# Performance work log

Hardware: AMD Instinct MI355X
Metric: run time of the kernel (lower is better)

## Reference

```python
import jax, jax.numpy as jnp
import numpy as np

B, H, W, C = 16, 56, 56, 384
NH, WIN = 8, 7
HD2 = C // NH // 2  # per-head k/v dim (=24)
SCALE = HD2 ** -0.5

def _ln(x, w, b, eps=1e-6):
    m = x.mean(-1, keepdims=True)
    v = ((x - m) ** 2).mean(-1, keepdims=True)
    return (x - m) / jnp.sqrt(v + eps) * w + b

def _dwconv(x, w, b):
    # x: [B,C,H,W], w: [C,1,7,7], groups=C depthwise, padding 3
    y = jax.lax.conv_general_dilated(x, w, (1, 1), [(3, 3), (3, 3)],
        dimension_numbers=('NCHW', 'OIHW', 'NCHW'), feature_group_count=x.shape[1])
    return y + b[None, :, None, None]

def setup_inputs():
    key = jax.random.key(0)
    ks = iter(jax.random.split(key, 32))
    def lin(i, o):
        return jax.random.normal(next(ks), (i, o), jnp.float32) * 0.02
    C2 = C // 2
    return dict(
        x=jax.random.normal(next(ks), (B, H, W, C), jnp.float32),
        x_e=jax.random.normal(next(ks), (B, H, W, C2), jnp.float32),
        norm_w=jnp.ones((C,), jnp.float32), norm_b=jnp.zeros((C,), jnp.float32),
        norme_w=jnp.ones((C2,), jnp.float32), norme_b=jnp.zeros((C2,), jnp.float32),
        q_w=lin(C, C), q_b=jnp.zeros((C,), jnp.float32),
        qcut_w=lin(C, C2), qcut_b=jnp.zeros((C2,), jnp.float32),
        a_w=lin(C, C), a_b=jnp.zeros((C,), jnp.float32),
        l_w=lin(C, C), l_b=jnp.zeros((C,), jnp.float32),
        conv_w=jax.random.normal(next(ks), (C, 1, 7, 7), jnp.float32) * 0.02,
        conv_b=jnp.zeros((C,), jnp.float32),
        econv_w=jax.random.normal(next(ks), (C2, 1, 7, 7), jnp.float32) * 0.02,
        econv_b=jnp.zeros((C2,), jnp.float32),
        efore_w=lin(C2, C2), efore_b=jnp.zeros((C2,), jnp.float32),
        eback_w=lin(C2, C2), eback_b=jnp.zeros((C2,), jnp.float32),
        kv_w=lin(C, C), kv_b=jnp.zeros((C,), jnp.float32),
        scl_w=lin(3 * C2, C2), scl_b=jnp.zeros((C2,), jnp.float32),
        proj_w=lin(2 * C, C), proj_b=jnp.zeros((C,), jnp.float32),
        proje_w=lin(2 * C, C2), proje_b=jnp.zeros((C2,), jnp.float32),
    )

def reference(x, x_e, norm_w, norm_b, norme_w, norme_b, q_w, q_b, qcut_w, qcut_b,
              a_w, a_b, l_w, l_b, conv_w, conv_b, econv_w, econv_b,
              efore_w, efore_b, eback_w, eback_b, kv_w, kv_b, scl_w, scl_b,
              proj_w, proj_b, proje_w, proje_b):
    C2 = C // 2
    xn = _ln(x, norm_w, norm_b)
    xen = _ln(x_e, norme_w, norme_b)
    # pooled shortcut queries: AdaptiveAvgPool2d((7,7)) == uniform 8x8 mean since H=W=56
    sc = jnp.concatenate([xn, xen], -1).transpose(0, 3, 1, 2)          # [B,3C/2,H,W]
    pooled = sc.reshape(B, 3 * C2, WIN, H // WIN, WIN, W // WIN).mean((3, 5))
    pooled = pooled.transpose(0, 2, 3, 1)                               # [B,7,7,3C/2]
    m = (pooled @ scl_w + scl_b).reshape(B, WIN * WIN, NH, HD2).transpose(0, 2, 1, 3)
    q = xn @ q_w + q_b
    cut = xn @ qcut_w + qcut_b
    lx = jax.nn.gelu(xn @ l_w + l_b, approximate=False)                 # [B,H,W,C]
    a = _dwconv(lx.transpose(0, 3, 1, 2), conv_w, conv_b).transpose(0, 2, 3, 1) @ a_w + a_b
    kv = (lx.reshape(B, H * W, C) @ kv_w + kv_b).reshape(B, H * W, 2, NH, HD2)
    k = kv[:, :, 0].transpose(0, 2, 1, 3)                               # [B,NH,HW,HD2]
    v = kv[:, :, 1].transpose(0, 2, 1, 3)
    p = jax.nn.softmax(jnp.einsum('bnqd,bnkd->bnqk', m * SCALE, k), -1) # [B,NH,49,HW]
    o = jnp.einsum('bnqk,bnkd->bnqd', p, v)                             # [B,NH,49,HD2]
    o = o.reshape(B, NH, WIN, WIN, HD2).transpose(0, 1, 4, 2, 3).reshape(B, C2, WIN, WIN)
    attn = jax.image.resize(o, (B, C2, H, W), method='bilinear').transpose(0, 2, 3, 1)
    # x_e depthwise branch
    ef = xen @ efore_w + efore_b
    xe2 = _dwconv(ef.transpose(0, 3, 1, 2), econv_w, econv_b).transpose(0, 2, 3, 1) @ eback_w + eback_b
    cut = cut * xe2
    g = q * a
    cat = jnp.concatenate([g, attn, cut], -1)                           # [B,H,W,2C]
    x_e_out = cat @ proje_w + proje_b
    x_out = cat @ proj_w + proj_b
    return (x_out, x_e_out)
```

## Files before the change

### kernel.cpp

```cpp
#include <hip/hip_runtime.h>
#include <math.h>

#define NB 16
#define NHW 3136
#define NROWS 50176
#define CD 384
#define CH2 192
#define SCL 0.20412414523193154f

typedef short bf16x8 __attribute__((ext_vector_type(8)));
typedef float f32x4 __attribute__((ext_vector_type(4)));
typedef unsigned short ushort;

static __device__ __forceinline__ float gelu_exact(float v) {
  return 0.5f * v * (1.0f + erff(v * 0.70710678118654752440f));
}
static __device__ __forceinline__ ushort f2bf(float f) {
  unsigned u = __builtin_bit_cast(unsigned, f);
  u += 0x7fffu + ((u >> 16) & 1u);
  return (ushort)(u >> 16);
}
static __device__ __forceinline__ float bf2f(ushort h) {
  unsigned u = ((unsigned)h) << 16;
  return __builtin_bit_cast(float, u);
}

template<int CN>
__global__ __launch_bounds__(256) void ln_k(const float* __restrict__ x,
    const float* __restrict__ w, const float* __restrict__ b,
    ushort* __restrict__ oh, ushort* __restrict__ ol)
{
  constexpr int NPER = CN / 64;
  int wave = threadIdx.x >> 6, lane = threadIdx.x & 63;
  int row = blockIdx.x * 4 + wave;
  const float* xp = x + (size_t)row * CN;
  float v[NPER];
  float s = 0.f;
  #pragma unroll
  for (int i = 0; i < NPER; i++) { v[i] = xp[lane + 64*i]; s += v[i]; }
  #pragma unroll
  for (int off = 32; off; off >>= 1) s += __shfl_xor(s, off);
  float mean = s * (1.0f / CN);
  float vs = 0.f;
  #pragma unroll
  for (int i = 0; i < NPER; i++) { float d = v[i] - mean; vs += d*d; }
  #pragma unroll
  for (int off = 32; off; off >>= 1) vs += __shfl_xor(vs, off);
  float rstd = rsqrtf(vs * (1.0f / CN) + 1e-6f);
  #pragma unroll
  for (int i = 0; i < NPER; i++) {
    int c = lane + 64*i;
    float y = (v[i] - mean) * rstd * w[c] + b[c];
    ushort h = f2bf(y);
    oh[(size_t)row * CN + c] = h;
    ol[(size_t)row * CN + c] = f2bf(y - bf2f(h));
  }
}

__global__ __launch_bounds__(256) void wcvt_k(const float* __restrict__ W,
    int K, int N, ushort* __restrict__ Wh, ushort* __restrict__ Wl)
{
  __shared__ float tl[32][33];
  int k0 = blockIdx.x * 32, n0 = blockIdx.y * 32;
  int r = threadIdx.x >> 5, c = threadIdx.x & 31;
  #pragma unroll
  for (int i = 0; i < 4; i++) {
    int kk = r + 8*i;
    float v = (n0 + c < N) ? W[(size_t)(k0 + kk) * N + n0 + c] : 0.f;
    tl[kk][c] = v;
  }
  __syncthreads();
  #pragma unroll
  for (int i = 0; i < 4; i++) {
    int n = n0 + r + 8*i;
    float v = tl[c][r + 8*i];
    ushort h = f2bf(v);
    Wh[(size_t)n * K + k0 + c] = h;
    Wl[(size_t)n * K + k0 + c] = f2bf(v - bf2f(h));
  }
}

__global__ void pool_k(const ushort* __restrict__ xnh, const ushort* __restrict__ xnl,
                       const ushort* __restrict__ xeh, const ushort* __restrict__ xel,
                       float* __restrict__ pooled)
{
  int c = threadIdx.x;
  int blk = blockIdx.x;
  int b = blk / 49, q = blk % 49;
  int py = q / 7, px = q % 7;
  float s = 0.f;
  if (c < CD) {
    size_t base = (((size_t)(b*56 + py*8))*56 + px*8) * CD + c;
    #pragma unroll
    for (int iy = 0; iy < 8; iy++)
      for (int ix = 0; ix < 8; ix++) {
        size_t o = base + (size_t)(iy*56 + ix) * CD;
        s += bf2f(xnh[o]) + bf2f(xnl[o]);
      }
  } else {
    int cc = c - CD;
    size_t base = (((size_t)(b*56 + py*8))*56 + px*8) * CH2 + cc;
    #pragma unroll
    for (int iy = 0; iy < 8; iy++)
      for (int ix = 0; ix < 8; ix++) {
        size_t o = base + (size_t)(iy*56 + ix) * CH2;
        s += bf2f(xeh[o]) + bf2f(xel[o]);
      }
  }
  pooled[(size_t)blk * 576 + c] = s * (1.0f / 64.0f);
}

__global__ __launch_bounds__(256) void gemm_k(
    const float* __restrict__ A, int lda,
    const float* __restrict__ B, int ldb,
    const float* __restrict__ bias,
    float* __restrict__ C, int ldc,
    int M, int N, int K)
{
  __shared__ float As[16][128 + 4];
  __shared__ float Bs[16][64 + 4];
  const int tid = threadIdx.x;
  const int tx = tid & 15;
  const int ty = tid >> 4;
  const int mbase = blockIdx.y * 128;
  const int nbase = blockIdx.x * 64;
  float acc[8][4] = {};
  for (int k0 = 0; k0 < K; k0 += 16) {
    #pragma unroll
    for (int r = 0; r < 2; r++) {
      int idx = tid + r * 256;
      int m = idx >> 2;
      int kq = (idx & 3) * 4;
      float4 av = {0.f, 0.f, 0.f, 0.f};
      if (mbase + m < M)
        av = *reinterpret_cast<const float4*>(&A[(size_t)(mbase + m) * lda + k0 + kq]);
      As[kq + 0][m] = av.x; As[kq + 1][m] = av.y;
      As[kq + 2][m] = av.z; As[kq + 3][m] = av.w;
    }
    {
      int k = tid >> 4;
      int nq = (tid & 15) * 4;
      float4 bv = *reinterpret_cast<const float4*>(&B[(size_t)(k0 + k) * ldb + nbase + nq]);
      *reinterpret_cast<float4*>(&Bs[k][nq]) = bv;
    }
    __syncthreads();
    #pragma unroll
    for (int k = 0; k < 16; k++) {
      float a0[8], b0[4];
      #pragma unroll
      for (int i = 0; i < 8; i++) a0[i] = As[k][ty*8 + i];
      #pragma unroll
      for (int j = 0; j < 4; j++) b0[j] = Bs[k][tx*4 + j];
      #pragma unroll
      for (int i = 0; i < 8; i++)
        #pragma unroll
        for (int j = 0; j < 4; j++)
          acc[i][j] += a0[i] * b0[j];
    }
    __syncthreads();
  }
  float bv[4];
  #pragma unroll
  for (int j = 0; j < 4; j++) bv[j] = bias[nbase + tx*4 + j];
  #pragma unroll
  for (int i = 0; i < 8; i++) {
    int m = mbase + ty*8 + i;
    if (m < M) {
      float* cp = &C[(size_t)m * ldc + nbase + tx*4];
      #pragma unroll
      for (int j = 0; j < 4; j++) cp[j] = acc[i][j] + bv[j];
    }
  }
}

template<int FLAGS>
__global__ __launch_bounds__(256, 2) void gemm_f3(
    const ushort* __restrict__ Ah, const ushort* __restrict__ Al, int lda,
    const ushort* __restrict__ Bh, const ushort* __restrict__ Bl,
    const float* __restrict__ bias,
    float* __restrict__ Cf, ushort* __restrict__ Ch, ushort* __restrict__ Cl,
    int ldc, int N, int K)
{
  __shared__ __align__(16) ushort lds[4 * 8 * 64 * 8];
  const int t = threadIdx.x;
  const int lane = t & 63, wave = t >> 6;
  const int wm = wave >> 1, wn = wave & 1;
  const int mbase = blockIdx.x * 128, nbase = blockIdx.y * 128;
  const int r = t >> 2, kc = t & 3;

  f32x4 acc[4][4];
  #pragma unroll
  for (int i = 0; i < 4; i++)
    #pragma unroll
    for (int j = 0; j < 4; j++) acc[i][j] = (f32x4){0.f, 0.f, 0.f, 0.f};

  for (int k0 = 0; k0 < K; k0 += 32) {
    __syncthreads();
    #pragma unroll
    for (int p = 0; p < 2; p++) {
      const ushort* src = p ? Al : Ah;
      #pragma unroll
      for (int hh = 0; hh < 2; hh++) {
        int row = hh * 64 + r;
        bf16x8 v = *(const bf16x8*)(src + (size_t)(mbase + row) * lda + k0 + kc * 8);
        int f = row >> 4, l = (row & 15) + kc * 16;
        *(bf16x8*)&lds[((p * 8 + f) * 64 + l) * 8] = v;
      }
    }
    #pragma unroll
    for (int p = 0; p < 2; p++) {
      const ushort* src = p ? Bl : Bh;
      #pragma unroll
      for (int hh = 0; hh < 2; hh++) {
        int row = hh * 64 + r;
        bf16x8 v = *(const bf16x8*)(src + (size_t)(nbase + row) * K + k0 + kc * 8);
        int f = row >> 4, l = (row & 15) + kc * 16;
        *(bf16x8*)&lds[(((2 + p) * 8 + f) * 64 + l) * 8] = v;
      }
    }
    __syncthreads();
    bf16x8 ah[4], al_[4], bh[4], bl_[4];
    #pragma unroll
    for (int i = 0; i < 4; i++) {
      ah[i]  = *(const bf16x8*)&lds[((0 * 8 + wm * 4 + i) * 64 + lane) * 8];
      al_[i] = *(const bf16x8*)&lds[((1 * 8 + wm * 4 + i) * 64 + lane) * 8];
      bh[i]  = *(const bf16x8*)&lds[((2 * 8 + wn * 4 + i) * 64 + lane) * 8];
      bl_[i] = *(const bf16x8*)&lds[((3 * 8 + wn * 4 + i) * 64 + lane) * 8];
    }
    #pragma unroll
    for (int mi = 0; mi < 4; mi++)
      #pragma unroll
      for (int ni = 0; ni < 4; ni++) {
        acc[mi][ni] = __builtin_amdgcn_mfma_f32_16x16x32_bf16(ah[mi],  bh[ni],  acc[mi][ni], 0, 0, 0);
        acc[mi][ni] = __builtin_amdgcn_mfma_f32_16x16x32_bf16(ah[mi],  bl_[ni], acc[mi][ni], 0, 0, 0);
        acc[mi][ni] = __builtin_amdgcn_mfma_f32_16x16x32_bf16(al_[mi], bh[ni],  acc[mi][ni], 0, 0, 0);
      }
  }

  #pragma unroll
  for (int ni = 0; ni < 4; ni++) {
    int col = nbase + wn * 64 + ni * 16 + (lane & 15);
    if (col >= N) continue;
    float bv = bias[col];
    #pragma unroll
    for (int mi = 0; mi < 4; mi++) {
      int row0 = mbase + wm * 64 + mi * 16 + ((lane >> 4) << 2);
      #pragma unroll
      for (int rr = 0; rr < 4; rr++) {
        size_t off = (size_t)(row0 + rr) * ldc + col;
        float v = acc[mi][ni][rr] + bv;
        if (FLAGS & 2) v = (bf2f(Ch[off]) + bf2f(Cl[off])) * v;
        if (FLAGS & 1) v = gelu_exact(v);
        if (FLAGS & 4) {
          Cf[off] = v;
        } else {
          ushort h = f2bf(v);
          Ch[off] = h;
          Cl[off] = f2bf(v - bf2f(h));
        }
      }
    }
  }
}

template<int CH>
__global__ __launch_bounds__(256) void dwconv_k(const ushort* __restrict__ inh,
    const ushort* __restrict__ inl,
    const float* __restrict__ wgt, const float* __restrict__ bias,
    ushort* __restrict__ outh, ushort* __restrict__ outl)
{
  __shared__ float in_t[196 * 64];
  __shared__ float wlds[64 * 49];

  const int t = threadIdx.x;
  const int c = t & 63;
  const int pg = t >> 6;
  const int tile = blockIdx.x;
  const int cbase = blockIdx.y * 64;
  const int b = blockIdx.z;
  const int oy0 = (tile / 7) * 8;
  const int ox0 = (tile % 7) * 8;

  #pragma unroll 7
  for (int i = 0; i < 49; i++) {
    int p = pg + 4 * i;
    int iy = p / 14, ix = p % 14;
    int gy = oy0 + iy - 3;
    int gx = ox0 + ix - 3;
    float v = 0.f;
    if ((unsigned)gy < 56u && (unsigned)gx < 56u) {
      size_t gidx = ((size_t)(b * 56 + gy) * 56 + gx) * CH + cbase + c;
      v = bf2f(inh[gidx]) + bf2f(inl[gidx]);
    }
    in_t[p * 64 + c] = v;
  }
  #pragma unroll
  for (int i = 0; i < 13; i++) {
    int j = t + 256 * i;
    if (j < 64 * 49) wlds[j] = wgt[(size_t)cbase * 49 + j];
  }
  __syncthreads();

  float bv = bias[cbase + c];
  float acc[2][8];
  #pragma unroll
  for (int r = 0; r < 2; r++)
    #pragma unroll
    for (int x = 0; x < 8; x++) acc[r][x] = bv;

  #pragma unroll
  for (int dy = 0; dy < 7; dy++) {
    float wrow[7];
    #pragma unroll
    for (int dx = 0; dx < 7; dx++) wrow[dx] = wlds[c * 49 + dy * 7 + dx];
    #pragma unroll
    for (int r = 0; r < 2; r++) {
      int oy = pg * 2 + r;
      int iy = oy + dy;
      float win[14];
      #pragma unroll
      for (int j = 0; j < 14; j++) win[j] = in_t[(iy * 14 + j) * 64 + c];
      #pragma unroll
      for (int dx = 0; dx < 7; dx++)
        #pragma unroll
        for (int x = 0; x < 8; x++)
          acc[r][x] += win[x + dx] * wrow[dx];
    }
  }

  #pragma unroll
  for (int r = 0; r < 2; r++) {
    int oy = pg * 2 + r;
    #pragma unroll
    for (int x = 0; x < 8; x++) {
      size_t oidx = ((size_t)(b * 56 + oy0 + oy) * 56 + ox0 + x) * CH + cbase + c;
      float val = acc[r][x];
      ushort h = f2bf(val);
      outh[oidx] = h;
      outl[oidx] = f2bf(val - bf2f(h));
    }
  }
}

__global__ __launch_bounds__(256) void attn_part_k(const float* __restrict__ mbuf,
    const float* __restrict__ kv, float* __restrict__ part)
{
  __shared__ float red[4][64][26];
  int bh = blockIdx.x;
  int b = bh >> 3, h = bh & 7;
  int chunk = blockIdx.y;
  int wave = threadIdx.x >> 6, lane = threadIdx.x & 63;
  int qq = lane < 49 ? lane : 48;
  float mq[24];
  const float* mp = mbuf + ((size_t)(b*49 + qq)) * 192 + h * 24;
  #pragma unroll
  for (int d = 0; d < 24; d++) mq[d] = mp[d] * SCL;
  float mx = -1e30f, sm = 0.f, acc[24] = {};
  int k0 = chunk * 392 + wave * 98, k1 = k0 + 98;
  for (int key = k0; key < k1; key++) {
    const float* kp = kv + ((size_t)(b*NHW + key)) * 384 + h * 24;
    float s0 = 0.f, s1 = 0.f;
    #pragma unroll
    for (int d = 0; d < 24; d += 2) { s0 += mq[d] * kp[d]; s1 += mq[d+1] * kp[d+1]; }
    float s = s0 + s1;
    float nm = fmaxf(mx, s);
    float f = __expf(mx - nm);
    float p = __expf(s - nm);
    sm = sm * f + p;
    const float* vp = kp + 192;
    #pragma unroll
    for (int d = 0; d < 24; d++) acc[d] = acc[d] * f + p * vp[d];
    mx = nm;
  }
  red[wave][lane][0] = mx;
  red[wave][lane][1] = sm;
  #pragma unroll
  for (int d = 0; d < 24; d++) red[wave][lane][2 + d] = acc[d];
  __syncthreads();
  if (wave == 0 && lane < 49) {
    float gm = -1e30f, gs = 0.f, ga[24] = {};
    #pragma unroll
    for (int w = 0; w < 4; w++) {
      float wm = red[w][lane][0], wsm = red[w][lane][1];
      float nm = fmaxf(gm, wm);
      float f1 = __expf(gm - nm), f2 = __expf(wm - nm);
      gs = gs * f1 + wsm * f2;
      #pragma unroll
      for (int d = 0; d < 24; d++)
        ga[d] = ga[d] * f1 + red[w][lane][2 + d] * f2;
      gm = nm;
    }
    float* pp = part + ((size_t)(bh * 8 + chunk) * 49 + lane) * 26;
    pp[0] = gm; pp[1] = gs;
    #pragma unroll
    for (int d = 0; d < 24; d++) pp[2 + d] = ga[d];
  }
}

__global__ void attn_merge_k(const float* __restrict__ part, float* __restrict__ obuf)
{
  int bh = blockIdx.x;
  int b = bh >> 3, h = bh & 7;
  int lane = threadIdx.x;
  if (lane >= 49) return;
  float gm = -1e30f, gs = 0.f, ga[24] = {};
  #pragma unroll
  for (int c = 0; c < 8; c++) {
    const float* pp = part + ((size_t)(bh * 8 + c) * 49 + lane) * 26;
    float wm = pp[0], wsm = pp[1];
    float nm = fmaxf(gm, wm);
    float f1 = __expf(gm - nm), f2 = __expf(wm - nm);
    gs = gs * f1 + wsm * f2;
    #pragma unroll
    for (int d = 0; d < 24; d++) ga[d] = ga[d] * f1 + pp[2 + d] * f2;
    gm = nm;
  }
  float inv = 1.0f / gs;
  float* op = obuf + ((size_t)b * 192 + h * 24) * 49 + lane;
  #pragma unroll
  for (int d = 0; d < 24; d++) op[d * 49] = ga[d] * inv;
}

__global__ __launch_bounds__(256) void upsample_k(const float* __restrict__ obuf,
    ushort* __restrict__ cath, ushort* __restrict__ catl)
{
  int idx = blockIdx.x * 256 + threadIdx.x;
  if (idx >= NB * NHW * CH2) return;
  int c = idx % CH2;
  int pos = idx / CH2;
  int x = pos % 56, y = (pos / 56) % 56, b = pos / NHW;
  float sy = (y + 0.5f) * 0.125f - 0.5f;
  float sx = (x + 0.5f) * 0.125f - 0.5f;
  int y0 = (int)floorf(sy); float ty = sy - (float)y0;
  int x0 = (int)floorf(sx); float tx = sx - (float)x0;
  int y0c = max(y0, 0), y1c = min(y0 + 1, 6);
  int x0c = max(x0, 0), x1c = min(x0 + 1, 6);
  const float* ob = obuf + ((size_t)b * 192 + c) * 49;
  float v = (1.f - ty) * ((1.f - tx) * ob[y0c*7 + x0c] + tx * ob[y0c*7 + x1c])
          +        ty  * ((1.f - tx) * ob[y1c*7 + x0c] + tx * ob[y1c*7 + x1c]);
  size_t off = (size_t)pos * 768 + 384 + c;
  ushort h = f2bf(v);
  cath[off] = h;
  catl[off] = f2bf(v - bf2f(h));
}

extern "C" void kernel_launch(void* const* d_in, const int* in_sizes, int n_in,
                              void* d_out, int out_size, void* d_ws, size_t ws_size,
                              hipStream_t stream) {
  const float* x       = (const float*)d_in[0];
  const float* x_e     = (const float*)d_in[1];
  const float* norm_w  = (const float*)d_in[2];
  const float* norm_b  = (const float*)d_in[3];
  const float* norme_w = (const float*)d_in[4];
  const float* norme_b = (const float*)d_in[5];
  const float* q_w     = (const float*)d_in[6];
  const float* q_b     = (const float*)d_in[7];
  const float* qcut_w  = (const float*)d_in[8];
  const float* qcut_b  = (const float*)d_in[9];
  const float* a_w     = (const float*)d_in[10];
  const float* a_b     = (const float*)d_in[11];
  const float* l_w     = (const float*)d_in[12];
  const float* l_b     = (const float*)d_in[13];
  const float* conv_w  = (const float*)d_in[14];
  const float* conv_b  = (const float*)d_in[15];
  const float* econv_w = (const float*)d_in[16];
  const float* econv_b = (const float*)d_in[17];
  const float* efore_w = (const float*)d_in[18];
  const float* efore_b = (const float*)d_in[19];
  const float* eback_w = (const float*)d_in[20];
  const float* eback_b = (const float*)d_in[21];
  const float* kv_w    = (const float*)d_in[22];
  const float* kv_b    = (const float*)d_in[23];
  const float* scl_w   = (const float*)d_in[24];
  const float* scl_b   = (const float*)d_in[25];
  const float* proj_w  = (const float*)d_in[26];
  const float* proj_b  = (const float*)d_in[27];
  const float* proje_w = (const float*)d_in[28];
  const float* proje_b = (const float*)d_in[29];
  float* out = (float*)d_out;

  char* w8 = (char*)d_ws;
  const size_t P384B = (size_t)NROWS * 384 * 2;
  const size_t P192B = (size_t)NROWS * 192 * 2;
  const size_t P768B = (size_t)NROWS * 768 * 2;
  size_t o = 0;
  auto alloc = [&](size_t bytes) { size_t r = o; o += (bytes + 255) & ~(size_t)255; return r; };
  size_t xnh_o  = alloc(P384B);
  size_t xnl_o  = alloc(P384B);
  size_t xenh_o = alloc(P192B);
  size_t xenl_o = alloc(P192B);
  size_t lxh_o  = alloc(P384B);
  size_t lxl_o  = alloc(P384B);
  size_t cath_o = alloc(P768B);
  size_t catl_o = alloc(P768B);
  size_t pooled_o = alloc(784 * 576 * 4);
  size_t mbuf_o   = alloc(784 * 192 * 4);
  size_t obuf_o   = alloc((size_t)NB * 192 * 49 * 4);
  size_t part_o   = alloc((size_t)128 * 8 * 49 * 26 * 4);
  size_t qwh_o  = alloc(384 * 384 * 2), qwl_o  = alloc(384 * 384 * 2);
  size_t qcwh_o = alloc(256 * 384 * 2), qcwl_o = alloc(256 * 384 * 2);
  size_t lwh_o  = alloc(384 * 384 * 2), lwl_o  = alloc(384 * 384 * 2);
  size_t awh_o  = alloc(384 * 384 * 2), awl_o  = alloc(384 * 384 * 2);
  size_t kvwh_o = alloc(384 * 384 * 2), kvwl_o = alloc(384 * 384 * 2);
  size_t efwh_o = alloc(256 * 192 * 2), efwl_o = alloc(256 * 192 * 2);
  size_t ebwh_o = alloc(256 * 192 * 2), ebwl_o = alloc(256 * 192 * 2);
  size_t pjwh_o = alloc(384 * 768 * 2), pjwl_o = alloc(384 * 768 * 2);
  size_t pjewh_o = alloc(256 * 768 * 2), pjewl_o = alloc(256 * 768 * 2);

  auto U = [&](size_t off) { return (ushort*)(w8 + off); };
  auto F = [&](size_t off) { return (float*)(w8 + off); };

  ushort *xnh = U(xnh_o), *xnl = U(xnl_o), *xenh = U(xenh_o), *xenl = U(xenl_o);
  ushort *lxh = U(lxh_o), *lxl = U(lxl_o);
  ushort *cath = U(cath_o), *catl = U(catl_o);
  float *pooled = F(pooled_o), *mbuf = F(mbuf_o), *obuf = F(obuf_o), *part = F(part_o);
  ushort *convh = xnh, *convl = xnl;
  float  *kvbuf = F(xnh_o);
  ushort *econvh = U(xnh_o), *econvl = U(xnh_o + P192B);
  ushort *efh = lxh, *efl = lxl;

  wcvt_k<<<dim3(12, 12), 256, 0, stream>>>(q_w,     384, 384, U(qwh_o),  U(qwl_o));
  wcvt_k<<<dim3(12,  8), 256, 0, stream>>>(qcut_w,  384, 192, U(qcwh_o), U(qcwl_o));
  wcvt_k<<<dim3(12, 12), 256, 0, stream>>>(l_w,     384, 384, U(lwh_o),  U(lwl_o));
  wcvt_k<<<dim3(12, 12), 256, 0, stream>>>(a_w,     384, 384, U(awh_o),  U(awl_o));
  wcvt_k<<<dim3(12, 12), 256, 0, stream>>>(kv_w,    384, 384, U(kvwh_o), U(kvwl_o));
  wcvt_k<<<dim3( 6,  8), 256, 0, stream>>>(efore_w, 192, 192, U(efwh_o), U(efwl_o));
  wcvt_k<<<dim3( 6,  8), 256, 0, stream>>>(eback_w, 192, 192, U(ebwh_o), U(ebwl_o));
  wcvt_k<<<dim3(24, 12), 256, 0, stream>>>(proj_w,  768, 384, U(pjwh_o), U(pjwl_o));
  wcvt_k<<<dim3(24,  8), 256, 0, stream>>>(proje_w, 768, 192, U(pjewh_o), U(pjewl_o));

  ln_k<384><<<NROWS/4, 256, 0, stream>>>(x,   norm_w,  norm_b,  xnh, xnl);
  ln_k<192><<<NROWS/4, 256, 0, stream>>>(x_e, norme_w, norme_b, xenh, xenl);
  pool_k<<<NB*49, 576, 0, stream>>>(xnh, xnl, xenh, xenl, pooled);
  gemm_k<<<dim3(3, 7), 256, 0, stream>>>(pooled, 576, scl_w, 192, scl_b,
                                         mbuf, 192, 784, 192, 576);
  gemm_f3<0><<<dim3(392, 3), 256, 0, stream>>>(xnh, xnl, 384, U(qwh_o), U(qwl_o), q_b,
                                               nullptr, cath, catl, 768, 384, 384);
  gemm_f3<0><<<dim3(392, 2), 256, 0, stream>>>(xnh, xnl, 384, U(qcwh_o), U(qcwl_o), qcut_b,
                                               nullptr, cath + 576, catl + 576, 768, 192, 384);
  gemm_f3<1><<<dim3(392, 3), 256, 0, stream>>>(xnh, xnl, 384, U(lwh_o), U(lwl_o), l_b,
                                               nullptr, lxh, lxl, 384, 384, 384);
  dwconv_k<384><<<dim3(49, 6, NB), 256, 0, stream>>>(lxh, lxl, conv_w, conv_b, convh, convl);
  gemm_f3<2><<<dim3(392, 3), 256, 0, stream>>>(convh, convl, 384, U(awh_o), U(awl_o), a_b,
                                               nullptr, cath, catl, 768, 384, 384);
  gemm_f3<4><<<dim3(392, 3), 256, 0, stream>>>(lxh, lxl, 384, U(kvwh_o), U(kvwl_o), kv_b,
                                               kvbuf, nullptr, nullptr, 384, 384, 384);
  attn_part_k<<<dim3(NB*8, 8), 256, 0, stream>>>(mbuf, kvbuf, part);
  attn_merge_k<<<NB*8, 64, 0, stream>>>(part, obuf);
  upsample_k<<<(NB*NHW*CH2)/256, 256, 0, stream>>>(obuf, cath, catl);
  gemm_f3<0><<<dim3(392, 2), 256, 0, stream>>>(xenh, xenl, 192, U(efwh_o), U(efwl_o), efore_b,
                                               nullptr, efh, efl, 192, 192, 192);
  dwconv_k<192><<<dim3(49, 3, NB), 256, 0, stream>>>(efh, efl, econv_w, econv_b, econvh, econvl);
  gemm_f3<2><<<dim3(392, 2), 256, 0, stream>>>(econvh, econvl, 192, U(ebwh_o), U(ebwl_o), eback_b,
                                               nullptr, cath + 576, catl + 576, 768, 192, 192);
  gemm_f3<4><<<dim3(392, 3), 256, 0, stream>>>(cath, catl, 768, U(pjwh_o), U(pjwl_o), proj_b,
                                               out, nullptr, nullptr, 384, 384, 768);
  gemm_f3<4><<<dim3(392, 2), 256, 0, stream>>>(cath, catl, 768, U(pjewh_o), U(pjewl_o), proje_b,
                                               out + (size_t)NROWS * 384, nullptr, nullptr, 192, 192, 768);
}
```

Baseline: 1.585 ms.

## Use direct global-to-LDS loads in GEMM and shrink dwconv channel tiles

The bf16x3 GEMM now stages its A/B hi/lo tiles with global_load_lds, which writes straight into shared memory and bypasses registers. Each wave loads one of the four operand planes, and the barrier moves to the end of the loop. The depthwise conv now processes 32 channels per block with one output row per thread group, doubling the grid to cut LDS use and registers per block. The risk is ordering: nothing explicitly waits for the async LDS loads to finish before __syncthreads, and the 32-channel conv tiles make narrower, less coalesced global accesses.

```diff
diff --git a/kernel.cpp b/kernel.cpp
--- a/kernel.cpp
+++ b/kernel.cpp
@@ -23,6 +23,11 @@
 static __device__ __forceinline__ float bf2f(ushort h) {
   unsigned u = ((unsigned)h) << 16;
   return __builtin_bit_cast(float, u);
+}
+static __device__ __forceinline__ void gload16(const ushort* g, ushort* l) {
+  __builtin_amdgcn_global_load_lds(
+      (const __attribute__((address_space(1))) unsigned int*)g,
+      (__attribute__((address_space(3))) unsigned int*)l, 16, 0, 0);
 }
 
 template<int CN>
@@ -186,7 +191,14 @@
   const int lane = t & 63, wave = t >> 6;
   const int wm = wave >> 1, wn = wave & 1;
   const int mbase = blockIdx.x * 128, nbase = blockIdx.y * 128;
-  const int r = t >> 2, kc = t & 3;
+
+  const ushort* src = (wave == 0) ? Ah : (wave == 1) ? Al : (wave == 2) ? Bh : Bl;
+  const int ldg = (wave < 2) ? lda : K;
+  const int tbase = (wave < 2) ? mbase : nbase;
+  const int srow = lane & 15;
+  const int skc = lane >> 4;
+  const ushort* gsrc0 = src + (size_t)(tbase + srow) * ldg + skc * 8;
+  ushort* ldst = lds + wave * 4096 + lane * 8;
 
   f32x4 acc[4][4];
   #pragma unroll
@@ -195,30 +207,12 @@
     for (int j = 0; j < 4; j++) acc[i][j] = (f32x4){0.f, 0.f, 0.f, 0.f};
 
   for (int k0 = 0; k0 < K; k0 += 32) {
+    const ushort* g = gsrc0 + k0;
+    #pragma unroll
+    for (int f = 0; f < 8; f++)
+      gload16(g + (size_t)(f * 16) * ldg, ldst + f * 512);
     __syncthreads();
-    #pragma unroll
-    for (int p = 0; p < 2; p++) {
-      const ushort* src = p ? Al : Ah;
-      #pragma unroll
-      for (int hh = 0; hh < 2; hh++) {
-        int row = hh * 64 + r;
-        bf16x8 v = *(const bf16x8*)(src + (size_t)(mbase + row) * lda + k0 + kc * 8);
-        int f = row >> 4, l = (row & 15) + kc * 16;
-        *(bf16x8*)&lds[((p * 8 + f) * 64 + l) * 8] = v;
-      }
-    }
-    #pragma unroll
-    for (int p = 0; p < 2; p++) {
-      const ushort* src = p ? Bl : Bh;
-      #pragma unroll
-      for (int hh = 0; hh < 2; hh++) {
-        int row = hh * 64 + r;
-        bf16x8 v = *(const bf16x8*)(src + (size_t)(nbase + row) * K + k0 + kc * 8);
-        int f = row >> 4, l = (row & 15) + kc * 16;
-        *(bf16x8*)&lds[(((2 + p) * 8 + f) * 64 + l) * 8] = v;
-      }
-    }
-    __syncthreads();
+
     bf16x8 ah[4], al_[4], bh[4], bl_[4];
     #pragma unroll
     for (int i = 0; i < 4; i++) {
@@ -235,6 +229,7 @@
         acc[mi][ni] = __builtin_amdgcn_mfma_f32_16x16x32_bf16(ah[mi],  bl_[ni], acc[mi][ni], 0, 0, 0);
         acc[mi][ni] = __builtin_amdgcn_mfma_f32_16x16x32_bf16(al_[mi], bh[ni],  acc[mi][ni], 0, 0, 0);
       }
+    __syncthreads();
   }
 
   #pragma unroll
@@ -269,76 +264,69 @@
     const float* __restrict__ wgt, const float* __restrict__ bias,
     ushort* __restrict__ outh, ushort* __restrict__ outl)
 {
-  __shared__ float in_t[196 * 64];
-  __shared__ float wlds[64 * 49];
+  __shared__ float in_t[196 * 32];
+  __shared__ float wlds[32 * 49];
 
   const int t = threadIdx.x;
-  const int c = t & 63;
-  const int pg = t >> 6;
+  const int c = t & 31;
+  const int s = t >> 5;
   const int tile = blockIdx.x;
-  const int cbase = blockIdx.y * 64;
+  const int cbase = blockIdx.y * 32;
   const int b = blockIdx.z;
   const int oy0 = (tile / 7) * 8;
   const int ox0 = (tile % 7) * 8;
 
-  #pragma unroll 7
-  for (int i = 0; i < 49; i++) {
-    int p = pg + 4 * i;
-    int iy = p / 14, ix = p % 14;
-    int gy = oy0 + iy - 3;
-    int gx = ox0 + ix - 3;
-    float v = 0.f;
-    if ((unsigned)gy < 56u && (unsigned)gx < 56u) {
-      size_t gidx = ((size_t)(b * 56 + gy) * 56 + gx) * CH + cbase + c;
-      v = bf2f(inh[gidx]) + bf2f(inl[gidx]);
-    }
-    in_t[p * 64 + c] = v;
-  }
-  #pragma unroll
-  for (int i = 0; i < 13; i++) {
+  #pragma unroll
+  for (int i = 0; i < 25; i++) {
+    int p = s + 8 * i;
+    if (p < 196) {
+      int iy = p / 14, ix = p % 14;
+      int gy = oy0 + iy - 3;
+      int gx = ox0 + ix - 3;
+      float v = 0.f;
+      if ((unsigned)gy < 56u && (unsigned)gx < 56u) {
+        size_t gidx = ((size_t)(b * 56 + gy) * 56 + gx) * CH + cbase + c;
+        v = bf2f(inh[gidx]) + bf2f(inl[gidx]);
+      }
+      in_t[p * 32 + c] = v;
+    }
+  }
+  #pragma unroll
+  for (int i = 0; i < 7; i++) {
     int j = t + 256 * i;
-    if (j < 64 * 49) wlds[j] = wgt[(size_t)cbase * 49 + j];
+    if (j < 32 * 49) wlds[j] = wgt[(size_t)cbase * 49 + j];
   }
   __syncthreads();
 
   float bv = bias[cbase + c];
-  float acc[2][8];
-  #pragma unroll
-  for (int r = 0; r < 2; r++)
-    #pragma unroll
-    for (int x = 0; x < 8; x++) acc[r][x] = bv;
-
+  float acc[8];
+  #pragma unroll
+  for (int x = 0; x < 8; x++) acc[x] = bv;
+
+  const int oy = s;
   #pragma unroll
   for (int dy = 0; dy < 7; dy++) {
     float wrow[7];
     #pragma unroll
     for (int dx = 0; dx < 7; dx++) wrow[dx] = wlds[c * 49 + dy * 7 + dx];
-    #pragma unroll
-    for (int r = 0; r < 2; r++) {
-      int oy = pg * 2 + r;
-      int iy = oy + dy;
-      float win[14];
-      #pragma unroll
-      for (int j = 0; j < 14; j++) win[j] = in_t[(iy * 14 + j) * 64 + c];
-      #pragma unroll
-      for (int dx = 0; dx < 7; dx++)
-        #pragma unroll
-        for (int x = 0; x < 8; x++)
-          acc[r][x] += win[x + dx] * wrow[dx];
-    }
-  }
-
-  #pragma unroll
-  for (int r = 0; r < 2; r++) {
-    int oy = pg * 2 + r;
-    #pragma unroll
-    for (int x = 0; x < 8; x++) {
-      size_t oidx = ((size_t)(b * 56 + oy0 + oy) * 56 + ox0 + x) * CH + cbase + c;
-      float val = acc[r][x];
-      ushort h = f2bf(val);
-      outh[oidx] = h;
-      outl[oidx] = f2bf(val - bf2f(h));
-    }
+    int iy = oy + dy;
+    float win[14];
+    #pragma unroll
+    for (int j = 0; j < 14; j++) win[j] = in_t[(iy * 14 + j) * 32 + c];
+    #pragma unroll
+    for (int dx = 0; dx < 7; dx++)
+      #pragma unroll
+      for (int x = 0; x < 8; x++)
+        acc[x] += win[x + dx] * wrow[dx];
+  }
+
+  #pragma unroll
+  for (int x = 0; x < 8; x++) {
+    size_t oidx = ((size_t)(b * 56 + oy0 + oy) * 56 + ox0 + x) * CH + cbase + c;
+    float val = acc[x];
+    ushort h = f2bf(val);
+    outh[oidx] = h;
+    outl[oidx] = f2bf(val - bf2f(h));
   }
 }
 
@@ -540,7 +528,7 @@
                                                nullptr, cath + 576, catl + 576, 768, 192, 384);
   gemm_f3<1><<<dim3(392, 3), 256, 0, stream>>>(xnh, xnl, 384, U(lwh_o), U(lwl_o), l_b,
                                                nullptr, lxh, lxl, 384, 384, 384);
-  dwconv_k<384><<<dim3(49, 6, NB), 256, 0, stream>>>(lxh, lxl, conv_w, conv_b, convh, convl);
+  dwconv_k<384><<<dim3(49, 12, NB), 256, 0, stream>>>(lxh, lxl, conv_w, conv_b, convh, convl);
   gemm_f3<2><<<dim3(392, 3), 256, 0, stream>>>(convh, convl, 384, U(awh_o), U(awl_o), a_b,
                                                nullptr, cath, catl, 768, 384, 384);
   gemm_f3<4><<<dim3(392, 3), 256, 0, stream>>>(lxh, lxl, 384, U(kvwh_o), U(kvwl_o), kv_b,
@@ -550,7 +538,7 @@
   upsample_k<<<(NB*NHW*CH2)/256, 256, 0, stream>>>(obuf, cath, catl);
   gemm_f3<0><<<dim3(392, 2), 256, 0, stream>>>(xenh, xenl, 192, U(efwh_o), U(efwl_o), efore_b,
                                                nullptr, efh, efl, 192, 192, 192);
-  dwconv_k<192><<<dim3(49, 3, NB), 256, 0, stream>>>(efh, efl, econv_w, econv_b, econvh, econvl);
+  dwconv_k<192><<<dim3(49, 6, NB), 256, 0, stream>>>(efh, efl, econv_w, econv_b, econvh, econvl);
   gemm_f3<2><<<dim3(392, 2), 256, 0, stream>>>(econvh, econvl, 192, U(ebwh_o), U(ebwl_o), eback_b,
                                                nullptr, cath + 576, catl + 576, 768, 192, 192);
   gemm_f3<4><<<dim3(392, 3), 256, 0, stream>>>(cath, catl, 768, U(pjwh_o), U(pjwl_o), proj_b,
```

Measured after the change: 1.590 ms. Within noise of the previous version (+0.3%).
